# Kernel tuning notes

Hardware: AMD Instinct MI355X
Metric: run time of the kernel (lower is better)

## Reference

```python
import jax, jax.numpy as jnp
import numpy as np

B, S, F_IN, H, F_OUT, BB = 128, 1024, 128, 256, 128, 256


def setup_inputs() -> dict:
    key = jax.random.key(0)
    ks = jax.random.split(key, 16)
    s_in = 1.0 / np.sqrt(F_IN + H)
    s_bb = 1.0 / np.sqrt(BB)
    s_h = 1.0 / np.sqrt(H)
    return {
        "x": jax.random.normal(ks[0], (B, S, F_IN), dtype=jnp.float32),
        "ts": jax.random.uniform(ks[1], (B, S), dtype=jnp.float32),
        # backbone (depth=1): Linear(F_IN+H -> BB)
        "Wb": jax.random.normal(ks[2], (F_IN + H, BB), dtype=jnp.float32) * s_in,
        "bb": jnp.zeros((BB,), jnp.float32),
        # CfC heads: ff1, ff2, time_a, time_b (BB -> H)
        "Wff1": jax.random.normal(ks[3], (BB, H), dtype=jnp.float32) * s_bb,
        "bff1": jnp.zeros((H,), jnp.float32),
        "Wff2": jax.random.normal(ks[4], (BB, H), dtype=jnp.float32) * s_bb,
        "bff2": jnp.zeros((H,), jnp.float32),
        "Wta": jax.random.normal(ks[5], (BB, H), dtype=jnp.float32) * s_bb,
        "bta": jnp.zeros((H,), jnp.float32),
        "Wtb": jax.random.normal(ks[6], (BB, H), dtype=jnp.float32) * s_bb,
        "btb": jnp.zeros((H,), jnp.float32),
        # output projection Linear(H -> F_OUT)
        "Wout": jax.random.normal(ks[7], (H, F_OUT), dtype=jnp.float32) * s_h,
        "bout": jnp.zeros((F_OUT,), jnp.float32),
    }


def reference(x, ts, Wb, bb, Wff1, bff1, Wff2, bff2, Wta, bta, Wtb, btb, Wout, bout):
    # x: [B,S,F_IN], ts: [B,S] -> out: [B,S,F_OUT]
    batch = x.shape[0]
    hidden = Wff1.shape[1]

    def step(h, inp):
        xt, tt = inp  # xt: [B,F_IN], tt: [B]
        z = jnp.tanh(jnp.concatenate([xt, h], axis=-1) @ Wb + bb)  # backbone [B,BB]
        ff1 = jnp.tanh(z @ Wff1 + bff1)
        ff2 = jnp.tanh(z @ Wff2 + bff2)
        t_a = z @ Wta + bta
        t_b = z @ Wtb + btb
        t_interp = jax.nn.sigmoid(t_a * tt[:, None] + t_b)  # time-dependent gate
        h_new = ff1 * (1.0 - t_interp) + t_interp * ff2
        y = h_new @ Wout + bout
        return h_new, y

    h0 = jnp.zeros((batch, hidden), dtype=x.dtype)
    xs = (jnp.swapaxes(x, 0, 1), jnp.swapaxes(ts, 0, 1))  # time-major for scan
    _, ys = jax.lax.scan(step, h0, xs)  # ys: [S,B,F_OUT]
    return jnp.swapaxes(ys, 0, 1)
```

## Files before the change

### kernel.cpp

```cpp
#include <hip/hip_runtime.h>

#define Bn   128
#define Sn   1024
#define FIN  128
#define Hn   256
#define FOUT 128
#define KBB  384
#define NT1  1024

#define NV 8
#define NL 9
#define DYN_SMEM (NL * 1024 * 8 * 2)

#define WB_OFF 0
#define W4_OFF 98304
#define WO_OFF 360448
#define WS_HALVES 393216
#define HBUF_OFF WS_HALVES
#define XC_OFF (HBUF_OFF + (size_t)Bn * Sn * Hn)
#define WS_SPLIT_BYTES ((size_t)(WS_HALVES + (size_t)Bn * Sn * Hn) * 2)
#define WS_FULL_BYTES ((XC_OFF + (size_t)Bn * Sn * Hn) * 2)

typedef _Float16 h2 __attribute__((ext_vector_type(2)));
typedef _Float16 h8 __attribute__((ext_vector_type(8)));

__device__ __forceinline__ float dot2f(h2 a, h2 b, float c) {
#if __has_builtin(__builtin_amdgcn_fdot2)
  return __builtin_amdgcn_fdot2(a, b, c, false);
#else
  return c + (float)a[0] * (float)b[0] + (float)a[1] * (float)b[1];
#endif
}
__device__ __forceinline__ void dot8_4(h8 v, h8 w, float& c0, float& c1, float& c2, float& c3) {
  h2 v0 = {v[0], v[1]}, v1 = {v[2], v[3]}, v2 = {v[4], v[5]}, v3 = {v[6], v[7]};
  h2 w0 = {w[0], w[1]}, w1 = {w[2], w[3]}, w2 = {w[4], w[5]}, w3 = {w[6], w[7]};
  c0 = dot2f(v0, w0, c0); c1 = dot2f(v1, w1, c1);
  c2 = dot2f(v2, w2, c2); c3 = dot2f(v3, w3, c3);
}

__global__ __launch_bounds__(256) void pack_w(
    const float* __restrict__ Wb, const float* __restrict__ W1,
    const float* __restrict__ W2, const float* __restrict__ W3,
    const float* __restrict__ W4, const float* __restrict__ Wo,
    _Float16* __restrict__ ws) {
  int p = blockIdx.x * 256 + threadIdx.x;
  if (p >= WS_HALVES) return;
  float v;
  if (p < W4_OFF) {
    int r = p & 7, j = (p >> 3) & 255;
    int k = ((p >> 11) << 3) | r;
    v = Wb[k * 256 + j];
  } else if (p < WO_OFF) {
    int q = p - W4_OFF;
    int r = q & 7, j = (q >> 3) & 1023;
    int k = ((q >> 13) << 3) | r;
    int jj = j & 255;
    const float* Ws = (j < 256) ? W1 : (j < 512) ? W2 : (j < 768) ? W3 : W4;
    v = Ws[k * 256 + jj];
  } else {
    int q = p - WO_OFF;
    int r = q & 7, j = (q >> 3) & 127;
    int k = ((q >> 10) << 3) | r;
    v = Wo[k * 128 + j];
  }
  ws[p] = (_Float16)v;
}

__global__ __launch_bounds__(256) void xgemm(
    const float* __restrict__ x, const _Float16* __restrict__ ws,
    _Float16* __restrict__ xc) {
  __shared__ __align__(16) _Float16 sX[64 * 128];
  const int tid = threadIdx.x;
  const size_t r0 = (size_t)blockIdx.x * 64;
  const float* xb = x + r0 * 128;
#pragma unroll
  for (int m = 0; m < 32; ++m)
    sX[m * 256 + tid] = (_Float16)xb[m * 256 + tid];
  const _Float16* gX = ws + WB_OFF + (size_t)tid * 8;
  h8 wx[16];
#pragma unroll
  for (int L = 0; L < 16; ++L) wx[L] = *(const h8*)(gX + (size_t)L * 2048);
  __syncthreads();
  for (int r = 0; r < 64; ++r) {
    float c0 = 0.f, c1 = 0.f, c2 = 0.f, c3 = 0.f;
#pragma unroll
    for (int L = 0; L < 16; ++L) {
      h8 v = *(const h8*)&sX[r * 128 + L * 8];
      dot8_4(v, wx[L], c0, c1, c2, c3);
    }
    xc[(r0 + r) * 256 + tid] = (_Float16)(c0 + c1 + c2 + c3);
  }
}

template <int XC, int INLINE_Y>
__global__ __launch_bounds__(NT1, 4) void cfc3(
    const float* __restrict__ x, const float* __restrict__ ts,
    const float* __restrict__ bb, const float* __restrict__ bf1,
    const float* __restrict__ bf2, const float* __restrict__ bta,
    const float* __restrict__ btb, const float* __restrict__ bo,
    _Float16* __restrict__ ws, float* __restrict__ out) {
  __shared__ __align__(16) _Float16 xh[KBB];
  __shared__ __align__(16) _Float16 zf[Hn];
  __shared__ float tsb[Sn];
  __shared__ float scrZ[768];
  __shared__ float scrH[768];
  __shared__ float scrY[896];
  extern __shared__ _Float16 sWH[];

  const int tid = threadIdx.x;
  const int b = blockIdx.x;
  const _Float16* Wb_p = ws + WB_OFF;
  const _Float16* W4_p = ws + W4_OFF;
  const _Float16* Wo_p = ws + WO_OFF;
  _Float16* hbuf = ws + HBUF_OFF;
  const _Float16* xcp = ws + XC_OFF;

  const float* xrow  = x  + (size_t)b * Sn * FIN;
  const float* tsrow = ts + (size_t)b * Sn;
  float*       orow  = out + (size_t)b * Sn * FOUT;

  const int jq = tid & 255;
  const int kw = tid >> 8;
  const float bbj = (tid < 256) ? bb[tid] : 0.f;
  const float bH = (kw == 0 ? bf1 : kw == 1 ? bf2 : kw == 2 ? bta : btb)[jq];
  const int jY = tid & 127, kq = tid >> 7;
  const float boj = (tid < 128) ? bo[tid] : 0.f;

  const _Float16* gZ = XC
      ? Wb_p + (size_t)(16 + kw * 8) * 2048 + (size_t)jq * 8
      : Wb_p + (size_t)(kw * 12) * 2048 + (size_t)jq * 8;
  const _Float16* gH = W4_p + (size_t)tid * 8;
  const _Float16* gY = Wo_p + ((size_t)(kq * 4) * 128 + jY) * 8;

  h8 wH[NV];
#pragma unroll
  for (int c = 0; c < NV; ++c) wH[c] = *(const h8*)(gH + (size_t)c * 8192);
#pragma unroll
  for (int c = 0; c < NV; ++c) asm volatile("" : "+v"(wH[c]));
#pragma unroll
  for (int cc = 0; cc < NL; ++cc)
    *(h8*)(sWH + (size_t)cc * 8192 + tid * 8) =
        *(const h8*)(gH + (size_t)(NV + cc) * 8192);

  tsb[tid] = tsrow[tid];
  if (tid < 128) ((unsigned*)xh)[64 + tid] = 0;
  if (XC == 0 && tid < 64) {
    float2 xv = *(const float2*)(xrow + 2 * tid);
    h2 p; p[0] = (_Float16)xv.x; p[1] = (_Float16)xv.y;
    *(h2*)&xh[2 * tid] = p;
  }
  __syncthreads();

  for (int st = 0; st < Sn; ++st) {
    float xcv = 0.f;
    if (XC && tid < 256)
      xcv = (float)xcp[((size_t)b * Sn + st) * 256 + tid];

    float2 xv; xv.x = 0.f; xv.y = 0.f;
    if (XC == 0 && tid >= 960 && st + 1 < Sn)
      xv = *(const float2*)(xrow + (size_t)(st + 1) * FIN + 2 * (tid - 960));

    float a0 = 0.f, a1 = 0.f, a2 = 0.f, a3 = 0.f;
    if (XC) {
#pragma unroll 4
      for (int c = 0; c < 8; ++c) {
        h8 v = *(const h8*)&xh[128 + (kw * 8 + c) * 8];
        h8 w = *(const h8*)(gZ + (size_t)c * 2048);
        dot8_4(v, w, a0, a1, a2, a3);
      }
    } else {
#pragma unroll 4
      for (int c = 0; c < 12; ++c) {
        h8 v = *(const h8*)&xh[(kw * 12 + c) * 8];
        h8 w = *(const h8*)(gZ + (size_t)c * 2048);
        dot8_4(v, w, a0, a1, a2, a3);
      }
    }
    float zs = a0 + a1 + a2 + a3;
    if (tid >= 256) scrZ[tid - 256] = zs;
    __syncthreads();
    if (tid < 256) {
      float zp = zs + scrZ[tid] + scrZ[256 + tid] + scrZ[512 + tid] + bbj;
      if (XC) zp += xcv;
      zf[tid] = (_Float16)tanhf(zp);
    }
    if (XC == 0 && tid >= 960 && st + 1 < Sn) {
      h2 p; p[0] = (_Float16)xv.x; p[1] = (_Float16)xv.y;
      *(h2*)&xh[2 * (tid - 960)] = p;
    }
    __syncthreads();

    float s0 = 0.f, s1 = 0.f, s2 = 0.f, s3 = 0.f;
#pragma unroll 2
    for (int c = NV + NL; c < 32; ++c) {
      h8 v = *(const h8*)&zf[c * 8];
      h8 w = *(const h8*)(gH + (size_t)c * 8192);
      dot8_4(v, w, s0, s1, s2, s3);
    }
    float b0 = 0.f, b1 = 0.f, b2 = 0.f, b3 = 0.f;
#pragma unroll
    for (int c = 0; c < NV; ++c) {
      h8 v = *(const h8*)&zf[c * 8];
      dot8_4(v, wH[c], b0, b1, b2, b3);
    }
#pragma unroll
    for (int cc = 0; cc < NL; ++cc) {
      h8 v = *(const h8*)&zf[(NV + cc) * 8];
      h8 w = *(const h8*)(sWH + (size_t)cc * 8192 + tid * 8);
      dot8_4(v, w, b0, b1, b2, b3);
    }
    float g = (b0 + s0) + (b1 + s1) + (b2 + s2) + (b3 + s3) + bH;
    if (tid >= 256) scrH[tid - 256] = g;
    __syncthreads();
    if (tid < 256) {
      float ff2 = scrH[tid], ta = scrH[256 + tid], tb = scrH[512 + tid];
      float tt = tsb[st];
      float sg = 1.f / (1.f + __expf(-(ta * tt + tb)));
      float hn = tanhf(g) * (1.f - sg) + sg * tanhf(ff2);
      xh[128 + tid] = (_Float16)hn;
      if (!INLINE_Y)
        hbuf[((size_t)b * Sn + st) * Hn + tid] = (_Float16)hn;
    }
    __syncthreads();

    if (INLINE_Y) {
      float y0 = 0.f, y1 = 0.f, y2 = 0.f, y3 = 0.f;
#pragma unroll
      for (int c = 0; c < 4; ++c) {
        h8 v = *(const h8*)&xh[128 + (kq * 4 + c) * 8];
        h8 w = *(const h8*)(gY + (size_t)c * 1024);
        dot8_4(v, w, y0, y1, y2, y3);
      }
      float ys = y0 + y1 + y2 + y3;
      if (tid >= 128) scrY[tid - 128] = ys;
      __syncthreads();
      if (tid < 128) {
        float y = ys + boj;
#pragma unroll
        for (int p = 0; p < 7; ++p) y += scrY[128 * p + tid];
        orow[(size_t)st * FOUT + tid] = y;
      }
    }
  }
}

#define SMEMY (65536 + 4096)
extern "C" __global__ __launch_bounds__(256, 4)
void ygemm(const _Float16* __restrict__ ws, const float* __restrict__ bo,
           float* __restrict__ out) {
  extern __shared__ char ysm[];
  _Float16* sWo = (_Float16*)ysm;
  _Float16* sH  = (_Float16*)(ysm + 65536);
  const int tid = threadIdx.x;
  { const uint4* g = (const uint4*)(ws + WO_OFF);
    uint4* l = (uint4*)sWo;
#pragma unroll
    for (int i = 0; i < 16; ++i) l[tid + 256 * i] = g[tid + 256 * i]; }
  const _Float16* hb = ws + HBUF_OFF;
  const int row0 = blockIdx.x * 256;
  const int j = tid & 127, rh = tid >> 7;
  const float boj = bo[j];
  for (int it = 0; it < 32; ++it) {
    const int rbase = row0 + it * 8;
    __syncthreads();
    ((uint4*)sH)[tid] = ((const uint4*)(hb + (size_t)rbase * 256))[tid];
    __syncthreads();
#pragma unroll
    for (int rr = rh; rr < 8; rr += 2) {
      float y0 = 0.f, y1 = 0.f, y2 = 0.f, y3 = 0.f;
#pragma unroll 4
      for (int c = 0; c < 32; ++c) {
        h8 v = *(const h8*)&sH[rr * 256 + c * 8];
        h8 w = *(const h8*)&sWo[((size_t)c * 128 + j) * 8];
        dot8_4(v, w, y0, y1, y2, y3);
      }
      out[(size_t)(rbase + rr) * 128 + j] = y0 + y1 + y2 + y3 + boj;
    }
  }
}

extern "C" void kernel_launch(void* const* d_in, const int* in_sizes, int n_in,
                              void* d_out, int out_size, void* d_ws, size_t ws_size,
                              hipStream_t stream) {
  const float* x   = (const float*)d_in[0];
  const float* ts  = (const float*)d_in[1];
  const float* Wb  = (const float*)d_in[2];
  const float* bb  = (const float*)d_in[3];
  const float* W1  = (const float*)d_in[4];
  const float* bf1 = (const float*)d_in[5];
  const float* W2  = (const float*)d_in[6];
  const float* bf2 = (const float*)d_in[7];
  const float* W3  = (const float*)d_in[8];
  const float* bta = (const float*)d_in[9];
  const float* W4  = (const float*)d_in[10];
  const float* btb = (const float*)d_in[11];
  const float* Wo  = (const float*)d_in[12];
  const float* bo  = (const float*)d_in[13];
  float* out = (float*)d_out;
  _Float16* ws = (_Float16*)d_ws;

  pack_w<<<WS_HALVES / 256, 256, 0, stream>>>(Wb, W1, W2, W3, W4, Wo, ws);

  if (ws_size >= WS_FULL_BYTES) {
    xgemm<<<(Bn * Sn) / 64, 256, 0, stream>>>(x, ws, ws + XC_OFF);
    hipFuncSetAttribute((const void*)(cfc3<1, 0>),
                        hipFuncAttributeMaxDynamicSharedMemorySize, DYN_SMEM);
    cfc3<1, 0><<<Bn, NT1, DYN_SMEM, stream>>>(x, ts, bb, bf1, bf2, bta, btb, bo, ws, out);
    hipFuncSetAttribute((const void*)ygemm,
                        hipFuncAttributeMaxDynamicSharedMemorySize, SMEMY);
    ygemm<<<(Bn * Sn) / 256, 256, SMEMY, stream>>>(ws, bo, out);
  } else if (ws_size >= WS_SPLIT_BYTES) {
    hipFuncSetAttribute((const void*)(cfc3<0, 0>),
                        hipFuncAttributeMaxDynamicSharedMemorySize, DYN_SMEM);
    cfc3<0, 0><<<Bn, NT1, DYN_SMEM, stream>>>(x, ts, bb, bf1, bf2, bta, btb, bo, ws, out);
    hipFuncSetAttribute((const void*)ygemm,
                        hipFuncAttributeMaxDynamicSharedMemorySize, SMEMY);
    ygemm<<<(Bn * Sn) / 256, 256, SMEMY, stream>>>(ws, bo, out);
  } else {
    hipFuncSetAttribute((const void*)(cfc3<0, 1>),
                        hipFuncAttributeMaxDynamicSharedMemorySize, DYN_SMEM);
    cfc3<0, 1><<<Bn, NT1, DYN_SMEM, stream>>>(x, ts, bb, bf1, bf2, bta, btb, bo, ws, out);
  }
}
```

Before: 4.972 ms.

## Halve recurrent block to 512 threads, each computing two gate outputs with more register-resident weights

The sequential recurrence kernel drops from 1024 to 512 threads per batch row, and each thread now accumulates two head outputs. Register caching of the fused head weights grows from 8 to 20 chunks per output (40 total), with one chunk in LDS and the rest streamed from global memory. The hidden-projection part of the backbone weights is also staged fully into LDS. Fewer threads mean cheaper block barriers and fewer cross-thread reduction partials per timestep, at the cost of very high register pressure and longer per-thread serial work.

New measurement: 4.162 ms. 16.3% less time.

```diff
diff --git a/kernel.cpp b/kernel.cpp
--- a/kernel.cpp
+++ b/kernel.cpp
@@ -6,11 +6,11 @@
 #define Hn   256
 #define FOUT 128
 #define KBB  384
-#define NT1  1024
-
-#define NV 8
-#define NL 9
-#define DYN_SMEM (NL * 1024 * 8 * 2)
+#define NT1  512
+
+#define NR4 20
+#define NL4 1
+#define DYN_SMEM ((32 * 256 * 8 + NL4 * 1024 * 8) * 2)
 
 #define WB_OFF 0
 #define W4_OFF 98304
@@ -93,7 +93,7 @@
 }
 
 template <int XC, int INLINE_Y>
-__global__ __launch_bounds__(NT1, 4) void cfc3(
+__global__ __launch_bounds__(NT1, 2) void cfc5(
     const float* __restrict__ x, const float* __restrict__ ts,
     const float* __restrict__ bb, const float* __restrict__ bf1,
     const float* __restrict__ bf2, const float* __restrict__ bta,
@@ -102,10 +102,11 @@
   __shared__ __align__(16) _Float16 xh[KBB];
   __shared__ __align__(16) _Float16 zf[Hn];
   __shared__ float tsb[Sn];
-  __shared__ float scrZ[768];
-  __shared__ float scrH[768];
-  __shared__ float scrY[896];
-  extern __shared__ _Float16 sWH[];
+  __shared__ float scrZ[256];
+  __shared__ float scrH[512];
+  extern __shared__ __align__(16) _Float16 dyn[];
+  _Float16* sWb  = dyn;
+  _Float16* sW4L = dyn + 32 * 256 * 8;
 
   const int tid = threadIdx.x;
   const int b = blockIdx.x;
@@ -119,35 +120,43 @@
   const float* tsrow = ts + (size_t)b * Sn;
   float*       orow  = out + (size_t)b * Sn * FOUT;
 
-  const int jq = tid & 255;
-  const int kw = tid >> 8;
+  const int jz = tid & 255, kz = tid >> 8;
   const float bbj = (tid < 256) ? bb[tid] : 0.f;
-  const float bH = (kw == 0 ? bf1 : kw == 1 ? bf2 : kw == 2 ? bta : btb)[jq];
-  const int jY = tid & 127, kq = tid >> 7;
-  const float boj = (tid < 128) ? bo[tid] : 0.f;
-
-  const _Float16* gZ = XC
-      ? Wb_p + (size_t)(16 + kw * 8) * 2048 + (size_t)jq * 8
-      : Wb_p + (size_t)(kw * 12) * 2048 + (size_t)jq * 8;
-  const _Float16* gH = W4_p + (size_t)tid * 8;
-  const _Float16* gY = Wo_p + ((size_t)(kq * 4) * 128 + jY) * 8;
-
-  h8 wH[NV];
-#pragma unroll
-  for (int c = 0; c < NV; ++c) wH[c] = *(const h8*)(gH + (size_t)c * 8192);
-#pragma unroll
-  for (int c = 0; c < NV; ++c) asm volatile("" : "+v"(wH[c]));
-#pragma unroll
-  for (int cc = 0; cc < NL; ++cc)
-    *(h8*)(sWH + (size_t)cc * 8192 + tid * 8) =
-        *(const h8*)(gH + (size_t)(NV + cc) * 8192);
-
-  tsb[tid] = tsrow[tid];
+  const float bHA = (tid < 256) ? bf1[tid] : bf2[tid - 256];
+  const float bHB = (tid < 256) ? bta[tid] : btb[tid - 256];
+  const int jY = tid & 127, kqY = tid >> 7;
+  const float boj = bo[jY];
+
+  if (XC) {
+    const h8* src = (const h8*)(Wb_p + (size_t)16 * 2048);
+    h8* dst = (h8*)sWb;
+    for (int i = tid; i < 8192; i += NT1) dst[i] = src[i];
+  }
+  {
+    const h8* src = (const h8*)(W4_p + (size_t)NR4 * 8192);
+    h8* dst = (h8*)sW4L;
+    for (int i = tid; i < NL4 * 1024; i += NT1) dst[i] = src[i];
+  }
+  for (int i = tid; i < Sn; i += NT1) tsb[i] = tsrow[i];
   if (tid < 128) ((unsigned*)xh)[64 + tid] = 0;
-  if (XC == 0 && tid < 64) {
+  if (!XC && tid < 64) {
     float2 xv = *(const float2*)(xrow + 2 * tid);
     h2 p; p[0] = (_Float16)xv.x; p[1] = (_Float16)xv.y;
     *(h2*)&xh[2 * tid] = p;
+  }
+
+  const _Float16* gA = W4_p + (size_t)tid * 8;
+  const _Float16* gB = W4_p + (size_t)(tid + 512) * 8;
+  h8 wA[NR4], wBv[NR4];
+#pragma unroll
+  for (int c = 0; c < NR4; ++c) {
+    wA[c]  = *(const h8*)(gA + (size_t)c * 8192);
+    wBv[c] = *(const h8*)(gB + (size_t)c * 8192);
+  }
+#pragma unroll
+  for (int c = 0; c < NR4; ++c) {
+    asm volatile("" : "+v"(wA[c]));
+    asm volatile("" : "+v"(wBv[c]));
   }
   __syncthreads();
 
@@ -155,68 +164,78 @@
     float xcv = 0.f;
     if (XC && tid < 256)
       xcv = (float)xcp[((size_t)b * Sn + st) * 256 + tid];
-
     float2 xv; xv.x = 0.f; xv.y = 0.f;
-    if (XC == 0 && tid >= 960 && st + 1 < Sn)
-      xv = *(const float2*)(xrow + (size_t)(st + 1) * FIN + 2 * (tid - 960));
+    if (!XC && tid >= 448 && st + 1 < Sn)
+      xv = *(const float2*)(xrow + (size_t)(st + 1) * FIN + 2 * (tid - 448));
 
     float a0 = 0.f, a1 = 0.f, a2 = 0.f, a3 = 0.f;
     if (XC) {
 #pragma unroll 4
-      for (int c = 0; c < 8; ++c) {
-        h8 v = *(const h8*)&xh[128 + (kw * 8 + c) * 8];
+      for (int c = 0; c < 16; ++c) {
+        int kc = kz * 16 + c;
+        h8 v = *(const h8*)&xh[128 + kc * 8];
+        h8 w = *(const h8*)&sWb[((size_t)kc * 256 + jz) * 8];
+        dot8_4(v, w, a0, a1, a2, a3);
+      }
+    } else {
+      const _Float16* gZ = Wb_p + ((size_t)(kz * 24) * 256 + jz) * 8;
+#pragma unroll 4
+      for (int c = 0; c < 24; ++c) {
+        h8 v = *(const h8*)&xh[(kz * 24 + c) * 8];
         h8 w = *(const h8*)(gZ + (size_t)c * 2048);
         dot8_4(v, w, a0, a1, a2, a3);
       }
-    } else {
-#pragma unroll 4
-      for (int c = 0; c < 12; ++c) {
-        h8 v = *(const h8*)&xh[(kw * 12 + c) * 8];
-        h8 w = *(const h8*)(gZ + (size_t)c * 2048);
-        dot8_4(v, w, a0, a1, a2, a3);
-      }
     }
     float zs = a0 + a1 + a2 + a3;
-    if (tid >= 256) scrZ[tid - 256] = zs;
+    if (kz) scrZ[jz] = zs;
     __syncthreads();
     if (tid < 256) {
-      float zp = zs + scrZ[tid] + scrZ[256 + tid] + scrZ[512 + tid] + bbj;
+      float zp = zs + scrZ[tid] + bbj;
       if (XC) zp += xcv;
       zf[tid] = (_Float16)tanhf(zp);
     }
-    if (XC == 0 && tid >= 960 && st + 1 < Sn) {
+    if (!XC && tid >= 448 && st + 1 < Sn) {
       h2 p; p[0] = (_Float16)xv.x; p[1] = (_Float16)xv.y;
-      *(h2*)&xh[2 * (tid - 960)] = p;
-    }
-    __syncthreads();
-
-    float s0 = 0.f, s1 = 0.f, s2 = 0.f, s3 = 0.f;
+      *(h2*)&xh[2 * (tid - 448)] = p;
+    }
+    __syncthreads();
+
+    float hA0 = 0.f, hA1 = 0.f, hA2 = 0.f, hA3 = 0.f;
+    float hB0 = 0.f, hB1 = 0.f, hB2 = 0.f, hB3 = 0.f;
 #pragma unroll 2
-    for (int c = NV + NL; c < 32; ++c) {
+    for (int c = NR4 + NL4; c < 32; ++c) {
+      h8 v  = *(const h8*)&zf[c * 8];
+      h8 wa = *(const h8*)(gA + (size_t)c * 8192);
+      h8 wb = *(const h8*)(gB + (size_t)c * 8192);
+      dot8_4(v, wa, hA0, hA1, hA2, hA3);
+      dot8_4(v, wb, hB0, hB1, hB2, hB3);
+    }
+#pragma unroll
+    for (int c = 0; c < NR4; ++c) {
       h8 v = *(const h8*)&zf[c * 8];
-      h8 w = *(const h8*)(gH + (size_t)c * 8192);
-      dot8_4(v, w, s0, s1, s2, s3);
-    }
-    float b0 = 0.f, b1 = 0.f, b2 = 0.f, b3 = 0.f;
-#pragma unroll
-    for (int c = 0; c < NV; ++c) {
-      h8 v = *(const h8*)&zf[c * 8];
-      dot8_4(v, wH[c], b0, b1, b2, b3);
-    }
-#pragma unroll
-    for (int cc = 0; cc < NL; ++cc) {
-      h8 v = *(const h8*)&zf[(NV + cc) * 8];
-      h8 w = *(const h8*)(sWH + (size_t)cc * 8192 + tid * 8);
-      dot8_4(v, w, b0, b1, b2, b3);
-    }
-    float g = (b0 + s0) + (b1 + s1) + (b2 + s2) + (b3 + s3) + bH;
-    if (tid >= 256) scrH[tid - 256] = g;
+      dot8_4(v, wA[c],  hA0, hA1, hA2, hA3);
+      dot8_4(v, wBv[c], hB0, hB1, hB2, hB3);
+    }
+#pragma unroll
+    for (int l = 0; l < NL4; ++l) {
+      h8 v  = *(const h8*)&zf[(NR4 + l) * 8];
+      h8 wa = *(const h8*)&sW4L[((size_t)l * 1024 + tid) * 8];
+      h8 wb = *(const h8*)&sW4L[((size_t)l * 1024 + tid + 512) * 8];
+      dot8_4(v, wa, hA0, hA1, hA2, hA3);
+      dot8_4(v, wb, hB0, hB1, hB2, hB3);
+    }
+    float gAv = hA0 + hA1 + hA2 + hA3 + bHA;
+    float gBv = hB0 + hB1 + hB2 + hB3 + bHB;
+    if (tid >= 256) {
+      scrH[tid - 256]       = gAv;
+      scrH[256 + tid - 256] = gBv;
+    }
     __syncthreads();
     if (tid < 256) {
-      float ff2 = scrH[tid], ta = scrH[256 + tid], tb = scrH[512 + tid];
+      float ff2v = scrH[tid], tbv = scrH[256 + tid];
       float tt = tsb[st];
-      float sg = 1.f / (1.f + __expf(-(ta * tt + tb)));
-      float hn = tanhf(g) * (1.f - sg) + sg * tanhf(ff2);
+      float sg = 1.f / (1.f + __expf(-(gBv * tt + tbv)));
+      float hn = tanhf(gAv) * (1.f - sg) + sg * tanhf(ff2v);
       xh[128 + tid] = (_Float16)hn;
       if (!INLINE_Y)
         hbuf[((size_t)b * Sn + st) * Hn + tid] = (_Float16)hn;
@@ -224,21 +243,20 @@
     __syncthreads();
 
     if (INLINE_Y) {
+      const _Float16* gY = Wo_p + ((size_t)(kqY * 8) * 128 + jY) * 8;
       float y0 = 0.f, y1 = 0.f, y2 = 0.f, y3 = 0.f;
 #pragma unroll
-      for (int c = 0; c < 4; ++c) {
-        h8 v = *(const h8*)&xh[128 + (kq * 4 + c) * 8];
+      for (int c = 0; c < 8; ++c) {
+        h8 v = *(const h8*)&xh[128 + (kqY * 8 + c) * 8];
         h8 w = *(const h8*)(gY + (size_t)c * 1024);
         dot8_4(v, w, y0, y1, y2, y3);
       }
-      float ys = y0 + y1 + y2 + y3;
-      if (tid >= 128) scrY[tid - 128] = ys;
+      float ysv = y0 + y1 + y2 + y3;
+      if (kqY) scrH[(kqY - 1) * 128 + jY] = ysv;
       __syncthreads();
-      if (tid < 128) {
-        float y = ys + boj;
-#pragma unroll
-        for (int p = 0; p < 7; ++p) y += scrY[128 * p + tid];
-        orow[(size_t)st * FOUT + tid] = y;
+      if (kqY == 0) {
+        float y = ysv + boj + scrH[jY] + scrH[128 + jY] + scrH[256 + jY];
+        orow[(size_t)st * FOUT + jY] = y;
       }
     }
   }
@@ -303,22 +321,22 @@
 
   if (ws_size >= WS_FULL_BYTES) {
     xgemm<<<(Bn * Sn) / 64, 256, 0, stream>>>(x, ws, ws + XC_OFF);
-    hipFuncSetAttribute((const void*)(cfc3<1, 0>),
+    hipFuncSetAttribute((const void*)(cfc5<1, 0>),
                         hipFuncAttributeMaxDynamicSharedMemorySize, DYN_SMEM);
-    cfc3<1, 0><<<Bn, NT1, DYN_SMEM, stream>>>(x, ts, bb, bf1, bf2, bta, btb, bo, ws, out);
+    cfc5<1, 0><<<Bn, NT1, DYN_SMEM, stream>>>(x, ts, bb, bf1, bf2, bta, btb, bo, ws, out);
     hipFuncSetAttribute((const void*)ygemm,
                         hipFuncAttributeMaxDynamicSharedMemorySize, SMEMY);
     ygemm<<<(Bn * Sn) / 256, 256, SMEMY, stream>>>(ws, bo, out);
   } else if (ws_size >= WS_SPLIT_BYTES) {
-    hipFuncSetAttribute((const void*)(cfc3<0, 0>),
+    hipFuncSetAttribute((const void*)(cfc5<0, 0>),
                         hipFuncAttributeMaxDynamicSharedMemorySize, DYN_SMEM);
-    cfc3<0, 0><<<Bn, NT1, DYN_SMEM, stream>>>(x, ts, bb, bf1, bf2, bta, btb, bo, ws, out);
+    cfc5<0, 0><<<Bn, NT1, DYN_SMEM, stream>>>(x, ts, bb, bf1, bf2, bta, btb, bo, ws, out);
     hipFuncSetAttribute((const void*)ygemm,
                         hipFuncAttributeMaxDynamicSharedMemorySize, SMEMY);
     ygemm<<<(Bn * Sn) / 256, 256, SMEMY, stream>>>(ws, bo, out);
   } else {
-    hipFuncSetAttribute((const void*)(cfc3<0, 1>),
+    hipFuncSetAttribute((const void*)(cfc5<0, 1>),
                         hipFuncAttributeMaxDynamicSharedMemorySize, DYN_SMEM);
-    cfc3<0, 1><<<Bn, NT1, DYN_SMEM, stream>>>(x, ts, bb, bf1, bf2, bta, btb, bo, ws, out);
-  }
-}
+    cfc5<0, 1><<<Bn, NT1, DYN_SMEM, stream>>>(x, ts, bb, bf1, bf2, bta, btb, bo, ws, out);
+  }
+}
```
